# Performance work log

Measured on AMD Instinct MI355X. Metric: run time of the kernel, lower is better.

## Reference

```python
import jax, jax.numpy as jnp
import numpy as np

SEQ_LEN = 4096
DIM = 256  # hidden_dim, must be even


def rope_tables(seq_len, dim):
    half = dim // 2
    pos = jnp.arange(seq_len, dtype=jnp.float32)[:, None]  # (s,1)
    div = jnp.exp(jnp.arange(half, dtype=jnp.float32) * (-jnp.log(jnp.float32(10000.0)) / half))
    ang = pos * div  # (s, half)
    return jnp.sin(ang), jnp.cos(ang)


def apply_rope(x, sin, cos):
    # x: (b, s, d); sin/cos: (s, d//2). Interleaved pair rotation.
    b, s, d = x.shape
    xp = x.reshape(b, s, d // 2, 2)
    x_even, x_odd = xp[..., 0], xp[..., 1]
    out_even = x_even * cos - x_odd * sin
    out_odd = x_even * sin + x_odd * cos
    return jnp.stack([out_even, out_odd], axis=-1).reshape(b, s, d)


def setup_inputs() -> dict:
    key = jax.random.key(0)
    k1, k2, k3, k4 = jax.random.split(key, 4)
    x = jax.random.normal(k1, (4, SEQ_LEN, DIM), dtype=jnp.float32)
    W0 = jax.random.normal(k2, (DIM, DIM), dtype=jnp.float32)
    W1 = jax.random.normal(k3, (DIM, DIM), dtype=jnp.float32)
    W2 = jax.random.normal(k4, (DIM, DIM), dtype=jnp.float32)
    return {"x": x, "W0": W0, "W1": W1, "W2": W2}


def reference(x, W0, W1, W2):
    sin, cos = rope_tables(x.shape[1], W0.shape[1])
    x0 = apply_rope(jnp.einsum('bsi,ih->bsh', x, W0), sin, cos)  # (b,s,h)
    x1 = apply_rope(jnp.einsum('bsi,ih->bsh', x, W1), sin, cos)  # (b,s,h)
    scores = jnp.einsum('bsh,bth->bst', x0, x1)                   # (b,s,s)
    attn = jax.nn.softmax(scores, axis=-1)
    x2 = jnp.einsum('bsh,ho->bso', x, W2)                         # (b,s,o)
    out = jnp.einsum('bst,bto->bso', attn, x2)
    return out[:, 0, :]
```

## Files before the change

### kernel.cpp

```cpp
#include <hip/hip_runtime.h>
#include <math.h>

#define BB 4
#define SS 4096
#define DD 256
#define WT_PLANE 65536

typedef __attribute__((ext_vector_type(8))) _Float16 h8v;
typedef __attribute__((ext_vector_type(4))) float f4v;

__device__ __forceinline__ ushort f2h(float f) {
    _Float16 h = (_Float16)f;
    return __builtin_bit_cast(ushort, h);
}
__device__ __forceinline__ float h2f(ushort u) {
    return (float)__builtin_bit_cast(_Float16, u);
}
__device__ __forceinline__ void split2htwo(float a, float b, uint& h, uint& l) {
    const ushort ah = f2h(a);
    const ushort al = f2h(a - h2f(ah));
    const ushort bh = f2h(b);
    const ushort bl = f2h(b - h2f(bh));
    h = (uint)ah | ((uint)bh << 16);
    l = (uint)al | ((uint)bl << 16);
}

__global__ __launch_bounds__(256) void prep_kernel(const float* __restrict__ x,
                                                   const float* __restrict__ W0,
                                                   const float* __restrict__ W1,
                                                   float* __restrict__ q,
                                                   float* __restrict__ out,
                                                   ushort* __restrict__ wt,
                                                   float* __restrict__ cs) {
    __shared__ float sh[64 * 65];
    const int bid = blockIdx.x;
    const int tid = threadIdx.x;

    if (bid < 2048) {
        const int t = ((bid & 63) << 6) | (tid & 63);
        const int j = ((bid >> 6) << 2) | (tid >> 6);
        const float kfac = (float)(-9.210340371976184 / 128.0);
        const float d = expf((float)j * kfac);
        float sv, cv;
        sincosf((float)t * d, &sv, &cv);
        *(float2*)(cs + ((size_t)j * SS + t) * 2) = make_float2(cv, sv);
    } else if (bid < 2080) {
        const int qb = bid - 2048;
        const int b = qb >> 3;
        const int hc = qb & 7;
        if (hc == 0) out[b * DD + tid] = 0.f;
        const int hk = tid & 31;
        const int iseg = tid >> 5;
        const int h = hc * 32 + hk;
        const float* xrow = x + (size_t)b * SS * DD;
        float p = 0.f;
#pragma unroll
        for (int k = 0; k < 32; ++k) {
            const int i = iseg * 32 + k;
            p = fmaf(xrow[i], W0[i * DD + h], p);
        }
        sh[tid] = p;
        __syncthreads();
        if (tid < 32) {
            float s = 0.f;
#pragma unroll
            for (int jj = 0; jj < 8; ++jj) s += sh[jj * 32 + tid];
            q[b * DD + hc * 32 + tid] = s;
        }
    } else {
        const int cb = bid - 2080;
        const int k0 = (cb & 3) * 64;
        const int c0 = (cb >> 2) * 64;
        {
            const int kr = tid >> 2;
            const int csg = tid & 3;
            const float* src = W1 + (size_t)(k0 + kr) * DD + c0 + csg * 16;
#pragma unroll
            for (int i = 0; i < 4; ++i) {
                const float4 v = *(const float4*)(src + i * 4);
                sh[kr * 65 + csg * 16 + i * 4 + 0] = v.x;
                sh[kr * 65 + csg * 16 + i * 4 + 1] = v.y;
                sh[kr * 65 + csg * 16 + i * 4 + 2] = v.z;
                sh[kr * 65 + csg * 16 + i * 4 + 3] = v.w;
            }
        }
        __syncthreads();
        {
            const int cr = tid >> 2;
            const int ks2 = tid & 3;
            const int c = c0 + cr;
#pragma unroll
            for (int oct = 0; oct < 2; ++oct) {
                const int k = k0 + ks2 * 16 + oct * 8;
                const int kl = ks2 * 16 + oct * 8;
                uint H[4], L[4];
#pragma unroll
                for (int i = 0; i < 4; ++i) {
                    const float fa = sh[(kl + 2 * i + 0) * 65 + cr];
                    const float fb = sh[(kl + 2 * i + 1) * 65 + cr];
                    split2htwo(fa, fb, H[i], L[i]);
                }
                const size_t idx = ((size_t)(c >> 4) * 8 + (k >> 5)) * 512
                                 + (size_t)((k >> 3) & 3) * 128 + (size_t)(c & 15) * 8;
                *(uint4*)(wt + idx) = make_uint4(H[0], H[1], H[2], H[3]);
                *(uint4*)(wt + WT_PLANE + idx) = make_uint4(L[0], L[1], L[2], L[3]);
            }
        }
    }
}

__global__ __launch_bounds__(1024, 4) void scores_mfma(const float* __restrict__ x,
                                                       const ushort* __restrict__ wt,
                                                       const float* __restrict__ q,
                                                       const float* __restrict__ cs,
                                                       float* __restrict__ scores,
                                                       float2* __restrict__ partials) {
    __shared__ __align__(16) unsigned char smem[65536];
    __shared__ float scomb[8][64];
    __shared__ float q_s[256];
    const int tid = threadIdx.x;
    const int bid = blockIdx.x;
    const int b = bid >> 6;
    const int row0 = (bid & 63) << 6;

    if (tid < 256) q_s[tid] = q[b * DD + tid];

    {
        const int r = tid >> 4;
        const int seg = tid & 15;
        const float* xr = x + ((size_t)(b * SS + row0 + r)) * DD + seg * 16;
        const int swz = (r & 15) << 4;
#pragma unroll
        for (int j = 0; j < 2; ++j) {
            const float4 f0 = *(const float4*)(xr + j * 8);
            const float4 f1 = *(const float4*)(xr + j * 8 + 4);
            uint H[4], L[4];
            split2htwo(f0.x, f0.y, H[0], L[0]);
            split2htwo(f0.z, f0.w, H[1], L[1]);
            split2htwo(f1.x, f1.y, H[2], L[2]);
            split2htwo(f1.z, f1.w, H[3], L[3]);
            const int s = seg * 2 + j;
            const int off = r * 512 + (((s << 4)) ^ swz);
            *(uint4*)(smem + off) = make_uint4(H[0], H[1], H[2], H[3]);
            *(uint4*)(smem + 32768 + off) = make_uint4(L[0], L[1], L[2], L[3]);
        }
    }
    __syncthreads();

    const int lane = tid & 63;
    const int wv = tid >> 6;
    const int rh = wv >> 3;
    const int cg = wv & 7;
    const int l15 = lane & 15;
    const int hg = lane >> 4;

    f4v acc[2][2];
#pragma unroll
    for (int rt = 0; rt < 2; ++rt)
#pragma unroll
        for (int ct = 0; ct < 2; ++ct) acc[rt][ct] = {0.f, 0.f, 0.f, 0.f};

    const ushort* wb = wt + (size_t)lane * 8;
    const int aswz = l15 << 4;

#pragma unroll
    for (int ks = 0; ks < 8; ++ks) {
        h8v a_h[2], a_l[2];
#pragma unroll
        for (int rt = 0; rt < 2; ++rt) {
            const int row = rh * 32 + rt * 16 + l15;
            const int off = row * 512 + ((((ks * 4 + hg) << 4)) ^ aswz);
            a_h[rt] = *(const h8v*)(smem + off);
            a_l[rt] = *(const h8v*)(smem + 32768 + off);
        }
#pragma unroll
        for (int ct = 0; ct < 2; ++ct) {
            const int gct = cg * 2 + ct;
            const ushort* bp = wb + (size_t)(gct * 8 + ks) * 512;
            const h8v b_h = *(const h8v*)(bp);
            const h8v b_l = *(const h8v*)(bp + WT_PLANE);
#pragma unroll
            for (int rt = 0; rt < 2; ++rt) {
                acc[rt][ct] = __builtin_amdgcn_mfma_f32_16x16x32_f16(a_h[rt], b_h, acc[rt][ct], 0, 0, 0);
                acc[rt][ct] = __builtin_amdgcn_mfma_f32_16x16x32_f16(a_h[rt], b_l, acc[rt][ct], 0, 0, 0);
                acc[rt][ct] = __builtin_amdgcn_mfma_f32_16x16x32_f16(a_l[rt], b_h, acc[rt][ct], 0, 0, 0);
            }
        }
    }

    const int par = l15 & 1;
    float p[2][4];
#pragma unroll
    for (int rt = 0; rt < 2; ++rt)
#pragma unroll
        for (int i = 0; i < 4; ++i) p[rt][i] = 0.f;

#pragma unroll
    for (int ct = 0; ct < 2; ++ct) {
        const int c = (cg * 2 + ct) * 16 + l15;
        const int j = c >> 1;
        const float qe = q_s[2 * j], qo = q_s[2 * j + 1];
        const float* csp = cs + (size_t)j * (SS * 2);
#pragma unroll
        for (int rt = 0; rt < 2; ++rt) {
            const int t0 = row0 + rh * 32 + rt * 16 + hg * 4;
            const float4 csA = *(const float4*)(csp + t0 * 2);
            const float4 csB = *(const float4*)(csp + t0 * 2 + 4);
            const float u0 = par ? (qo * csA.x - qe * csA.y) : (qe * csA.x + qo * csA.y);
            const float u1 = par ? (qo * csA.z - qe * csA.w) : (qe * csA.z + qo * csA.w);
            const float u2 = par ? (qo * csB.x - qe * csB.y) : (qe * csB.x + qo * csB.y);
            const float u3 = par ? (qo * csB.z - qe * csB.w) : (qe * csB.z + qo * csB.w);
            p[rt][0] = fmaf(acc[rt][ct][0], u0, p[rt][0]);
            p[rt][1] = fmaf(acc[rt][ct][1], u1, p[rt][1]);
            p[rt][2] = fmaf(acc[rt][ct][2], u2, p[rt][2]);
            p[rt][3] = fmaf(acc[rt][ct][3], u3, p[rt][3]);
        }
    }
#pragma unroll
    for (int rt = 0; rt < 2; ++rt) {
#pragma unroll
        for (int off = 1; off <= 8; off <<= 1) {
            p[rt][0] += __shfl_xor(p[rt][0], off);
            p[rt][1] += __shfl_xor(p[rt][1], off);
            p[rt][2] += __shfl_xor(p[rt][2], off);
            p[rt][3] += __shfl_xor(p[rt][3], off);
        }
        if (l15 == 0)
            *(float4*)&scomb[cg][rh * 32 + rt * 16 + hg * 4] =
                make_float4(p[rt][0], p[rt][1], p[rt][2], p[rt][3]);
    }
    __syncthreads();
    if (tid < 64) {
        float s = 0.f;
#pragma unroll
        for (int g = 0; g < 8; ++g) s += scomb[g][tid];
        scores[(size_t)b * SS + row0 + tid] = s;
        float m = s;
#pragma unroll
        for (int off = 32; off >= 1; off >>= 1) m = fmaxf(m, __shfl_xor(m, off));
        float sc = expf(s - m);
#pragma unroll
        for (int off = 32; off >= 1; off >>= 1) sc += __shfl_xor(sc, off);
        if (tid == 0) partials[(b << 6) + (bid & 63)] = make_float2(m, sc);
    }
}

__global__ __launch_bounds__(1024) void final_kernel(const float* __restrict__ x,
                                                     const float* __restrict__ scores,
                                                     const float2* __restrict__ partials,
                                                     const float* __restrict__ W2,
                                                     float* __restrict__ out) {
    const int c = blockIdx.x;
    const int b = blockIdx.y;
    const int tid = threadIdx.x;
    __shared__ float a_s[64];
    __shared__ float yls[4][256];
    __shared__ float MS[2];
    __shared__ int flag;
    if (tid == 0) flag = 0;

    if (tid < 64) {
        const float2 pp = partials[(b << 6) + tid];
        float m = pp.x;
#pragma unroll
        for (int off = 32; off >= 1; off >>= 1) m = fmaxf(m, __shfl_xor(m, off));
        float sc = pp.y * expf(pp.x - m);
#pragma unroll
        for (int off = 32; off >= 1; off >>= 1) sc += __shfl_xor(sc, off);
        if (tid == 0) {
            MS[0] = m;
            MS[1] = sc;
        }
    }
    __syncthreads();
    const float M = MS[0];
    const float inv = 1.0f / MS[1];

    if (tid < 64) {
        const float a = expf(scores[(size_t)b * SS + (c << 6) + tid] - M) * inv;
        a_s[tid] = a;
        if (__any(a != 0.f) && tid == 0) flag = 1;
    }
    __syncthreads();
    if (!flag) return;

    const int o = tid & 255;
    const int th = tid >> 8;
    float accv = 0.f;
#pragma unroll
    for (int t = th * 16; t < th * 16 + 16; ++t) {
        const float a = a_s[t];
        if (a != 0.f)
            accv = fmaf(a, x[((size_t)(b * SS + c * 64 + t)) * DD + o], accv);
    }
    yls[th][o] = accv;
    __syncthreads();

    float pr = 0.f;
#pragma unroll 8
    for (int ii = 0; ii < 64; ++ii) {
        const int i = th * 64 + ii;
        const float yv = ((yls[0][i] + yls[1][i]) + yls[2][i]) + yls[3][i];
        pr = fmaf(yv, W2[(size_t)i * DD + o], pr);
    }
    atomicAdd(&out[b * DD + o], pr);
}

extern "C" void kernel_launch(void* const* d_in, const int* in_sizes, int n_in,
                              void* d_out, int out_size, void* d_ws, size_t ws_size,
                              hipStream_t stream) {
    const float* x = (const float*)d_in[0];
    const float* W0 = (const float*)d_in[1];
    const float* W1 = (const float*)d_in[2];
    const float* W2 = (const float*)d_in[3];
    float* ws = (float*)d_ws;
    float* q = ws;
    float* scores = ws + 1024;
    float2* partials = (float2*)(ws + 17408);
    ushort* wt = (ushort*)(ws + 18432);
    float* cs = ws + 116736;
    float* out = (float*)d_out;

    prep_kernel<<<dim3(2096), 256, 0, stream>>>(x, W0, W1, q, out, wt, cs);
    scores_mfma<<<dim3(256), 1024, 0, stream>>>(x, wt, q, cs, scores, partials);
    final_kernel<<<dim3(64, BB), 1024, 0, stream>>>(x, scores, partials, W2, out);
}
```

Baseline: 28.35 us.

## Compute RoPE sin/cos tables in LDS inside scores kernel instead of prep

Removes the global cos/sin table that the prep kernel computed for all 4096 positions and 128 frequencies. Each scores block now computes only its 64 rows of cos/sin into a shared-memory buffer, and the epilogue reads them from LDS instead of global memory. The x loads are also issued earlier so they overlap with this computation. This shrinks the prep launch from 2096 blocks to 48 and drops the table's global write and read traffic. In exchange, each scores block repeats sincos work for its rows and uses about 66KB more LDS, which may limit occupancy.

```diff
diff --git a/kernel.cpp b/kernel.cpp
--- a/kernel.cpp
+++ b/kernel.cpp
@@ -30,24 +30,14 @@
                                                    const float* __restrict__ W1,
                                                    float* __restrict__ q,
                                                    float* __restrict__ out,
-                                                   ushort* __restrict__ wt,
-                                                   float* __restrict__ cs) {
+                                                   ushort* __restrict__ wt) {
     __shared__ float sh[64 * 65];
     const int bid = blockIdx.x;
     const int tid = threadIdx.x;
 
-    if (bid < 2048) {
-        const int t = ((bid & 63) << 6) | (tid & 63);
-        const int j = ((bid >> 6) << 2) | (tid >> 6);
-        const float kfac = (float)(-9.210340371976184 / 128.0);
-        const float d = expf((float)j * kfac);
-        float sv, cv;
-        sincosf((float)t * d, &sv, &cv);
-        *(float2*)(cs + ((size_t)j * SS + t) * 2) = make_float2(cv, sv);
-    } else if (bid < 2080) {
-        const int qb = bid - 2048;
-        const int b = qb >> 3;
-        const int hc = qb & 7;
+    if (bid < 32) {
+        const int b = bid >> 3;
+        const int hc = bid & 7;
         if (hc == 0) out[b * DD + tid] = 0.f;
         const int hk = tid & 31;
         const int iseg = tid >> 5;
@@ -68,7 +58,7 @@
             q[b * DD + hc * 32 + tid] = s;
         }
     } else {
-        const int cb = bid - 2080;
+        const int cb = bid - 32;
         const int k0 = (cb & 3) * 64;
         const int c0 = (cb >> 2) * 64;
         {
@@ -112,10 +102,10 @@
 __global__ __launch_bounds__(1024, 4) void scores_mfma(const float* __restrict__ x,
                                                        const ushort* __restrict__ wt,
                                                        const float* __restrict__ q,
-                                                       const float* __restrict__ cs,
                                                        float* __restrict__ scores,
                                                        float2* __restrict__ partials) {
     __shared__ __align__(16) unsigned char smem[65536];
+    __shared__ __align__(16) float cs_lds[128 * 132];
     __shared__ float scomb[8][64];
     __shared__ float q_s[256];
     const int tid = threadIdx.x;
@@ -123,27 +113,49 @@
     const int b = bid >> 6;
     const int row0 = (bid & 63) << 6;
 
+    const int r = tid >> 4;
+    const int seg = tid & 15;
+    const float* xr = x + ((size_t)(b * SS + row0 + r)) * DD + seg * 16;
+    float4 xf0 = *(const float4*)(xr);
+    float4 xf1 = *(const float4*)(xr + 4);
+    float4 xf2 = *(const float4*)(xr + 8);
+    float4 xf3 = *(const float4*)(xr + 12);
+
+    {
+        const float kfac = (float)(-9.210340371976184 / 128.0);
+        const int jj = tid >> 3;
+        const int tl0 = (tid & 7) * 8;
+        const float d = expf((float)jj * kfac);
+        float* dst = cs_lds + jj * 132 + tl0 * 2;
+#pragma unroll
+        for (int e = 0; e < 8; ++e) {
+            float sv, cv;
+            sincosf((float)(row0 + tl0 + e) * d, &sv, &cv);
+            dst[2 * e] = cv;
+            dst[2 * e + 1] = sv;
+        }
+    }
     if (tid < 256) q_s[tid] = q[b * DD + tid];
 
     {
-        const int r = tid >> 4;
-        const int seg = tid & 15;
-        const float* xr = x + ((size_t)(b * SS + row0 + r)) * DD + seg * 16;
         const int swz = (r & 15) << 4;
-#pragma unroll
-        for (int j = 0; j < 2; ++j) {
-            const float4 f0 = *(const float4*)(xr + j * 8);
-            const float4 f1 = *(const float4*)(xr + j * 8 + 4);
-            uint H[4], L[4];
-            split2htwo(f0.x, f0.y, H[0], L[0]);
-            split2htwo(f0.z, f0.w, H[1], L[1]);
-            split2htwo(f1.x, f1.y, H[2], L[2]);
-            split2htwo(f1.z, f1.w, H[3], L[3]);
-            const int s = seg * 2 + j;
-            const int off = r * 512 + (((s << 4)) ^ swz);
-            *(uint4*)(smem + off) = make_uint4(H[0], H[1], H[2], H[3]);
-            *(uint4*)(smem + 32768 + off) = make_uint4(L[0], L[1], L[2], L[3]);
-        }
+        uint H[4], L[4];
+        split2htwo(xf0.x, xf0.y, H[0], L[0]);
+        split2htwo(xf0.z, xf0.w, H[1], L[1]);
+        split2htwo(xf1.x, xf1.y, H[2], L[2]);
+        split2htwo(xf1.z, xf1.w, H[3], L[3]);
+        int s = seg * 2;
+        int off = r * 512 + (((s << 4)) ^ swz);
+        *(uint4*)(smem + off) = make_uint4(H[0], H[1], H[2], H[3]);
+        *(uint4*)(smem + 32768 + off) = make_uint4(L[0], L[1], L[2], L[3]);
+        split2htwo(xf2.x, xf2.y, H[0], L[0]);
+        split2htwo(xf2.z, xf2.w, H[1], L[1]);
+        split2htwo(xf3.x, xf3.y, H[2], L[2]);
+        split2htwo(xf3.z, xf3.w, H[3], L[3]);
+        s = seg * 2 + 1;
+        off = r * 512 + (((s << 4)) ^ swz);
+        *(uint4*)(smem + off) = make_uint4(H[0], H[1], H[2], H[3]);
+        *(uint4*)(smem + 32768 + off) = make_uint4(L[0], L[1], L[2], L[3]);
     }
     __syncthreads();
 
@@ -200,12 +212,12 @@
         const int c = (cg * 2 + ct) * 16 + l15;
         const int j = c >> 1;
         const float qe = q_s[2 * j], qo = q_s[2 * j + 1];
-        const float* csp = cs + (size_t)j * (SS * 2);
+        const float* csp = cs_lds + j * 132;
 #pragma unroll
         for (int rt = 0; rt < 2; ++rt) {
-            const int t0 = row0 + rh * 32 + rt * 16 + hg * 4;
-            const float4 csA = *(const float4*)(csp + t0 * 2);
-            const float4 csB = *(const float4*)(csp + t0 * 2 + 4);
+            const int tloc = rh * 32 + rt * 16 + hg * 4;
+            const float4 csA = *(const float4*)(csp + tloc * 2);
+            const float4 csB = *(const float4*)(csp + tloc * 2 + 4);
             const float u0 = par ? (qo * csA.x - qe * csA.y) : (qe * csA.x + qo * csA.y);
             const float u1 = par ? (qo * csA.z - qe * csA.w) : (qe * csA.z + qo * csA.w);
             const float u2 = par ? (qo * csB.x - qe * csB.y) : (qe * csB.x + qo * csB.y);
@@ -318,10 +330,9 @@
     float* scores = ws + 1024;
     float2* partials = (float2*)(ws + 17408);
     ushort* wt = (ushort*)(ws + 18432);
-    float* cs = ws + 116736;
     float* out = (float*)d_out;
 
-    prep_kernel<<<dim3(2096), 256, 0, stream>>>(x, W0, W1, q, out, wt, cs);
-    scores_mfma<<<dim3(256), 1024, 0, stream>>>(x, wt, q, cs, scores, partials);
+    prep_kernel<<<dim3(48), 256, 0, stream>>>(x, W0, W1, q, out, wt);
+    scores_mfma<<<dim3(256), 1024, 0, stream>>>(x, wt, q, scores, partials);
     final_kernel<<<dim3(64, BB), 1024, 0, stream>>>(x, scores, partials, W2, out);
 }
```

Measured after the change: 27.13 us. 4.3% less time.
